# Kernel optimization log

Hardware: AMD Instinct MI355X
Metric: run time of the kernel (lower is better)

The kernel has to match this reference:

```python
import jax, jax.numpy as jnp
import numpy as np

N_HEAD = 8
HEAD_DIM = 128
WINDOW = 512
ROPE_BASE = 10000.0


def _rope_tables(T, dtype):
    # inv_freq: [head_dim/2]
    inv_freq = 1.0 / (ROPE_BASE ** (jnp.arange(0, HEAD_DIM, 2, dtype=jnp.float32) / HEAD_DIM))
    t = jnp.arange(T, dtype=jnp.float32)
    freqs = jnp.einsum('i,j->ij', t, inv_freq)          # [T, head_dim/2]
    emb = jnp.concatenate([freqs, freqs], axis=-1)       # [T, head_dim]
    return jnp.cos(emb).astype(dtype), jnp.sin(emb).astype(dtype)


def _rotate_half(x):
    d = x.shape[-1] // 2
    return jnp.concatenate([-x[..., d:], x[..., :d]], axis=-1)


def setup_inputs() -> dict:
    key = jax.random.key(0)
    k1, k2, k3 = jax.random.split(key, 3)
    B, T, C = 2, 4096, 1024
    x = jax.random.normal(k1, (B, T, C), dtype=jnp.float32)
    w_qkv = jax.random.normal(k2, (3 * C, C), dtype=jnp.float32) * (1.0 / np.sqrt(C))
    w_o = jax.random.normal(k3, (C, C), dtype=jnp.float32) * (1.0 / np.sqrt(C))
    return {"x": x, "w_qkv": w_qkv, "w_o": w_o}


def reference(x, w_qkv, w_o):
    B, T, C = x.shape
    scale = 1.0 / np.sqrt(HEAD_DIM)
    qkv = x @ w_qkv.T                                     # [B,T,3C]
    q, k, v = jnp.split(qkv, 3, axis=-1)
    # [B, H, T, D]
    q = q.reshape(B, T, N_HEAD, HEAD_DIM).transpose(0, 2, 1, 3)
    k = k.reshape(B, T, N_HEAD, HEAD_DIM).transpose(0, 2, 1, 3)
    v = v.reshape(B, T, N_HEAD, HEAD_DIM).transpose(0, 2, 1, 3)
    cos, sin = _rope_tables(T, x.dtype)                   # [T, D]
    cos = cos[None, None]
    sin = sin[None, None]
    q = q * cos + _rotate_half(q) * sin
    k = k * cos + _rotate_half(k) * sin
    attn = jnp.einsum('bhqd,bhkd->bhqk', q, k) * scale    # [B,H,T,T]
    i = jnp.arange(T)[:, None]
    j = jnp.arange(T)[None, :]
    # causal (j<=i) AND sliding window triu(diag=-W) (j >= i - W)
    keep = (j <= i) & (j >= i - WINDOW)
    neg = jnp.finfo(attn.dtype).min
    attn = jnp.where(keep[None, None], attn, neg)
    attn = jax.nn.softmax(attn, axis=-1)
    out = jnp.einsum('bhqk,bhkd->bhqd', attn, v)          # [B,H,T,D]
    out = out.transpose(0, 2, 1, 3).reshape(B, T, C)
    return out @ w_o.T
```

## Files before the change

kernel.cpp:

```cpp
#include <hip/hip_runtime.h>
#include <hip/hip_bf16.h>

typedef unsigned short us;
typedef __attribute__((ext_vector_type(8))) __bf16 bf16x8;
typedef __attribute__((ext_vector_type(4))) float f32x4;

#define MFMA16(a, b, c) __builtin_amdgcn_mfma_f32_16x16x32_bf16(a, b, c, 0, 0, 0)

static __device__ __forceinline__ us f2bf(float f) {
  __hip_bfloat16 h = __float2bfloat16(f);
  return __builtin_bit_cast(us, h);
}

static __device__ __forceinline__ void gll16(const us* g, us* l) {
  __builtin_amdgcn_global_load_lds((const __attribute__((address_space(1))) void*)g,
                                   (__attribute__((address_space(3))) void*)l,
                                   16, 0, 0);
}

__global__ void prep_kernel(const float* __restrict__ x, const float* __restrict__ wq,
                            const float* __restrict__ wo, us* __restrict__ xb,
                            us* __restrict__ wqb, us* __restrict__ wob,
                            float* __restrict__ ct, float* __restrict__ st) {
  const int blk = blockIdx.x;
  const int tid = threadIdx.x;
  if (blk < 12288) {
    const float* in;
    us* out;
    int i;
    if (blk < 8192)      { in = x;  out = xb;  i = blk * 256 + tid; }
    else if (blk < 11264){ in = wq; out = wqb; i = (blk - 8192) * 256 + tid; }
    else                 { in = wo; out = wob; i = (blk - 11264) * 256 + tid; }
    float4 v = ((const float4*)in)[i];
    ushort4 o;
    o.x = f2bf(v.x); o.y = f2bf(v.y); o.z = f2bf(v.z); o.w = f2bf(v.w);
    ((ushort4*)out)[i] = o;
  } else {
    int i = (blk - 12288) * 256 + tid;
    int t = i >> 6, d = i & 63;
    float ang = (float)t * exp2f((float)d * -0.20762050593046014f);
    float s, c;
    sincosf(ang, &s, &c);
    ct[i] = c;
    st[i] = s;
  }
}

__global__ __launch_bounds__(256, 4)
void qkv_rope_kernel(const us* __restrict__ A, const us* __restrict__ B,
                     const float* __restrict__ ctab, const float* __restrict__ stab,
                     us* __restrict__ qb, us* __restrict__ kb, us* __restrict__ vtb) {
  __shared__ __align__(16) char smem_raw[128 * 136 * 2];
  us* sA = (us*)smem_raw;
  us* sB = sA + 128 * 64;
  us* sCus = (us*)smem_raw;

  const int tid = threadIdx.x;
  const int lane = tid & 63;
  const int wave = tid >> 6;
  const int l15 = lane & 15;
  const int lq = lane >> 4;
  const int m0 = blockIdx.x * 128;
  const int n0 = blockIdx.y * 128;
  const int wm = (wave & 1) * 64;
  const int wn2 = (wave >> 1) * 32;

  f32x4 acc[4][4] = {};

  for (int k0 = 0; k0 < 1024; k0 += 64) {
    for (int i = 0; i < 4; ++i) {
      int c = wave * 4 + i;
      int P = c * 64 + lane;
      int row = P >> 3;
      int cb = (P & 7) ^ (row & 7);
      gll16(A + (size_t)(m0 + row) * 1024 + k0 + cb * 8, sA + c * 512);
      gll16(B + (size_t)(n0 + row) * 1024 + k0 + cb * 8, sB + c * 512);
    }
    __syncthreads();
#pragma unroll
    for (int kk = 0; kk < 64; kk += 32) {
      const int cbr = (kk + lq * 8) >> 3;
      bf16x8 av[4], bv[4];
#pragma unroll
      for (int mt = 0; mt < 4; ++mt) {
        int m = wm + mt * 16 + l15;
        av[mt] = *(const bf16x8*)(sA + (m * 8 + (cbr ^ (m & 7))) * 8);
      }
#pragma unroll
      for (int nt = 0; nt < 4; ++nt) {
        int n = wn2 + (nt & 1) * 16 + (nt >> 1) * 64 + l15;
        bv[nt] = *(const bf16x8*)(sB + (n * 8 + (cbr ^ (n & 7))) * 8);
      }
#pragma unroll
      for (int mt = 0; mt < 4; ++mt)
#pragma unroll
        for (int nt = 0; nt < 4; ++nt)
          acc[mt][nt] = MFMA16(av[mt], bv[nt], acc[mt][nt]);
    }
    __syncthreads();
  }

  const int b = m0 >> 12;
  const int t0 = m0 & 4095;
  const int which = blockIdx.y >> 3;
  const int h = blockIdx.y & 7;

  if (which < 2) {
    us* outp = (which == 0) ? qb : kb;
    const size_t obase = ((size_t)(b * 8 + h)) * 4096 * 128;
#pragma unroll
    for (int mt = 0; mt < 4; ++mt)
#pragma unroll
      for (int r = 0; r < 4; ++r) {
        const int row = wm + mt * 16 + lq * 4 + r;
        const int tg = t0 + row;
        const float* cp = ctab + tg * 64 + wn2 + l15;
        const float* sp = stab + tg * 64 + wn2 + l15;
        const float c0 = cp[0], c1 = cp[16], s0 = sp[0], s1 = sp[16];
#pragma unroll
        for (int nt = 0; nt < 4; ++nt) {
          float xv = acc[mt][nt][r];
          float xp = acc[mt][nt ^ 2][r];
          float rot = (nt < 2) ? -xp : xp;
          float y = xv * ((nt & 1) ? c1 : c0) + rot * ((nt & 1) ? s1 : s0);
          sCus[row * 136 + wn2 + (nt & 1) * 16 + (nt >> 1) * 64 + l15] = f2bf(y);
        }
      }
    __syncthreads();
    for (int r = 0; r < 8; ++r) {
      int row = (tid >> 4) + r * 16;
      int col = (tid & 15) * 8;
      uint4 v = *(const uint4*)(sCus + row * 136 + col);
      *(uint4*)(outp + obase + (size_t)(t0 + row) * 128 + col) = v;
    }
  } else {
#pragma unroll
    for (int mt = 0; mt < 4; ++mt)
#pragma unroll
      for (int nt = 0; nt < 4; ++nt) {
        const int col = wn2 + (nt & 1) * 16 + (nt >> 1) * 64 + l15;
#pragma unroll
        for (int r = 0; r < 4; ++r)
          sCus[(wm + mt * 16 + lq * 4 + r) * 130 + col] = f2bf(acc[mt][nt][r]);
      }
    __syncthreads();
    for (int r = 0; r < 8; ++r) {
      int d = (tid >> 4) + r * 16;
      int tl0 = (tid & 15) * 8;
      union { us u[8]; uint4 v; } tmp;
#pragma unroll
      for (int j = 0; j < 8; ++j)
        tmp.u[j] = sCus[(tl0 + j) * 130 + d];
      *(uint4*)(vtb + ((size_t)((b * 8 + h) * 128 + d)) * 4096 + t0 + tl0) = tmp.v;
    }
  }
}

template <int MASK>
__device__ __forceinline__ void p_write(f32x4 (&s)[2][4], us* __restrict__ sP,
                                        int t0, int tj0, int wm2, int lq, int l15) {
  const float C2 = 0.08838834764831845f * 1.4426950408889634f;
#pragma unroll
  for (int mt = 0; mt < 2; ++mt)
#pragma unroll
    for (int nt = 0; nt < 4; ++nt) {
      const int jg = tj0 + nt * 16 + l15;
      const int cb = (nt * 16 + l15) >> 3;
      const int co = l15 & 7;
#pragma unroll
      for (int r = 0; r < 4; ++r) {
        const int rowl = wm2 + mt * 16 + lq * 4 + r;
        float v = s[mt][nt][r];
        if (MASK == 1) v = (jg + 512 >= t0 + rowl) ? v : -3.0e38f;
        if (MASK == 2) v = (jg <= t0 + rowl) ? v : -3.0e38f;
        sP[rowl * 64 + ((cb ^ (rowl & 7)) * 8) + co] = f2bf(exp2f(v * C2));
      }
    }
}

__global__ __launch_bounds__(256, 2)
void flash_kernel(const us* __restrict__ qg, const us* __restrict__ kg,
                  const us* __restrict__ vg, us* __restrict__ ao) {
  __shared__ us smem[40960];
  us* sK = smem;
  us* sV = smem + 16384;
  us* sP = smem + 32768;

  const int tid = threadIdx.x;
  const int lane = tid & 63;
  const int wave = tid >> 6;
  const int l15 = lane & 15;
  const int lq = lane >> 4;
  const int qx = blockIdx.x;
  const int h = blockIdx.y;
  const int b = blockIdx.z;
  const int t0 = qx * 128;
  const size_t bh = (size_t)(b * 8 + h);
  const int wm2 = wave * 32;

  bf16x8 qf[2][4];
#pragma unroll
  for (int mt = 0; mt < 2; ++mt)
#pragma unroll
    for (int ks = 0; ks < 4; ++ks)
      qf[mt][ks] = *(const bf16x8*)(qg + (bh * 4096 + t0 + wm2 + mt * 16 + l15) * 128 +
                                    ks * 32 + lq * 8);

  union { us u[8]; bf16x8 v; } one_u;
#pragma unroll
  for (int i = 0; i < 8; ++i) one_u.u[i] = 0x3F80;
  const bf16x8 vone = one_u.v;

  f32x4 o[2][9] = {};

  const int lo = t0 - 512;
  const int jtmin = (lo <= 0) ? 0 : (lo >> 6);
  const int jtmax = (t0 + 127) >> 6;
  const bool wmask = (t0 >= 512);

  auto stage = [&](int jt, int buf) {
    const int tj0 = jt * 64;
    us* dK = sK + buf * 8192;
    us* dV = sV + buf * 8192;
    for (int i = 0; i < 4; ++i) {
      int c = wave * 4 + i;
      int P = c * 64 + lane;
      int rowK = P >> 4;
      int cbK = (P & 15) ^ (rowK & 15);
      gll16(kg + (bh * 4096 + tj0 + rowK) * 128 + cbK * 8, dK + c * 512);
      int rowV = P >> 3;
      int cbV = (P & 7) ^ (rowV & 7);
      gll16(vg + (bh * 128 + rowV) * 4096 + tj0 + cbV * 8, dV + c * 512);
    }
  };

  stage(jtmin, 0);
  int cur = 0;

  for (int jt = jtmin; jt <= jtmax; ++jt) {
    __syncthreads();
    if (jt < jtmax) stage(jt + 1, cur ^ 1);

    const int tj0 = jt * 64;
    const us* sKc = sK + cur * 8192;
    const us* sVc = sV + cur * 8192;

    f32x4 s[2][4] = {};
#pragma unroll
    for (int ks = 0; ks < 4; ++ks) {
      const int cbr = ks * 4 + lq;
#pragma unroll
      for (int nt = 0; nt < 4; ++nt) {
        int n = nt * 16 + l15;
        bf16x8 bk = *(const bf16x8*)(sKc + (n * 16 + (cbr ^ (n & 15))) * 8);
#pragma unroll
        for (int mt = 0; mt < 2; ++mt)
          s[mt][nt] = MFMA16(qf[mt][ks], bk, s[mt][nt]);
      }
    }

    if (jt >= jtmax - 1)               p_write<2>(s, sP, t0, tj0, wm2, lq, l15);
    else if (wmask && jt <= jtmin + 1) p_write<1>(s, sP, t0, tj0, wm2, lq, l15);
    else                               p_write<0>(s, sP, t0, tj0, wm2, lq, l15);

#pragma unroll
    for (int ks = 0; ks < 2; ++ks) {
#pragma unroll
      for (int mt = 0; mt < 2; ++mt) {
        bf16x8 ap = *(const bf16x8*)(sP + (wm2 + mt * 16 + l15) * 64 +
                                     (((ks * 4 + lq) ^ (l15 & 7)) * 8));
#pragma unroll
        for (int dt = 0; dt < 8; ++dt) {
          int dd = dt * 16 + l15;
          bf16x8 bv = *(const bf16x8*)(sVc + (dd * 8 + ((ks * 4 + lq) ^ (dd & 7))) * 8);
          o[mt][dt] = MFMA16(ap, bv, o[mt][dt]);
        }
        o[mt][8] = MFMA16(ap, vone, o[mt][8]);
      }
    }
    cur ^= 1;
  }

#pragma unroll
  for (int mt = 0; mt < 2; ++mt)
#pragma unroll
    for (int r = 0; r < 4; ++r) {
      const float inv = 1.0f / o[mt][8][r];
      const int rowl = wm2 + mt * 16 + lq * 4 + r;
      const size_t base = ((size_t)b * 4096 + t0 + rowl) * 1024 + h * 128;
#pragma unroll
      for (int dt = 0; dt < 8; ++dt)
        ao[base + dt * 16 + l15] = f2bf(o[mt][dt][r] * inv);
    }
}

__global__ __launch_bounds__(256, 2)
void out_proj_kernel(const us* __restrict__ A, const us* __restrict__ B, float* __restrict__ C) {
  __shared__ us sA[128 * 64];
  __shared__ us sB[128 * 64];
  const int tid = threadIdx.x;
  const int lane = tid & 63;
  const int wave = tid >> 6;
  const int l15 = lane & 15;
  const int lq = lane >> 4;
  const int m0 = blockIdx.x * 128;
  const int n0 = blockIdx.y * 128;
  const int wm = (wave & 1) * 64;
  const int wn = (wave >> 1) * 64;
  f32x4 acc[4][4] = {};
  for (int k0 = 0; k0 < 1024; k0 += 64) {
    for (int i = 0; i < 4; ++i) {
      int c = wave * 4 + i;
      int P = c * 64 + lane;
      int row = P >> 3;
      int cb = (P & 7) ^ (row & 7);
      gll16(A + (size_t)(m0 + row) * 1024 + k0 + cb * 8, sA + c * 512);
      gll16(B + (size_t)(n0 + row) * 1024 + k0 + cb * 8, sB + c * 512);
    }
    __syncthreads();
#pragma unroll
    for (int kk = 0; kk < 64; kk += 32) {
      const int cbr = (kk + lq * 8) >> 3;
      bf16x8 av[4], bv[4];
#pragma unroll
      for (int mt = 0; mt < 4; ++mt) {
        int m = wm + mt * 16 + l15;
        av[mt] = *(const bf16x8*)(sA + (m * 8 + (cbr ^ (m & 7))) * 8);
      }
#pragma unroll
      for (int nt = 0; nt < 4; ++nt) {
        int n = wn + nt * 16 + l15;
        bv[nt] = *(const bf16x8*)(sB + (n * 8 + (cbr ^ (n & 7))) * 8);
      }
#pragma unroll
      for (int mt = 0; mt < 4; ++mt)
#pragma unroll
        for (int nt = 0; nt < 4; ++nt)
          acc[mt][nt] = MFMA16(av[mt], bv[nt], acc[mt][nt]);
    }
    __syncthreads();
  }
#pragma unroll
  for (int mt = 0; mt < 4; ++mt)
#pragma unroll
    for (int nt = 0; nt < 4; ++nt)
#pragma unroll
      for (int r = 0; r < 4; ++r)
        C[(size_t)(m0 + wm + mt * 16 + lq * 4 + r) * 1024 + (n0 + wn + nt * 16 + l15)] =
            acc[mt][nt][r];
}

extern "C" void kernel_launch(void* const* d_in, const int* in_sizes, int n_in,
                              void* d_out, int out_size, void* d_ws, size_t ws_size,
                              hipStream_t stream) {
  const float* x     = (const float*)d_in[0];
  const float* w_qkv = (const float*)d_in[1];
  const float* w_o   = (const float*)d_in[2];
  float* out = (float*)d_out;

  us* xb  = (us*)d_ws;
  us* wqb = xb  + (size_t)8192 * 1024;
  us* wob = wqb + (size_t)3072 * 1024;
  us* qb  = wob + (size_t)1024 * 1024;
  us* kb  = qb  + (size_t)2 * 8 * 4096 * 128;
  us* vtb = kb  + (size_t)2 * 8 * 4096 * 128;
  us* aob = vtb + (size_t)2 * 8 * 4096 * 128;
  float* ctab = (float*)(aob + (size_t)8192 * 1024);
  float* stab = ctab + (size_t)4096 * 64;

  prep_kernel<<<13312, 256, 0, stream>>>(x, w_qkv, w_o, xb, wqb, wob, ctab, stab);
  qkv_rope_kernel<<<dim3(64, 24), 256, 0, stream>>>(xb, wqb, ctab, stab, qb, kb, vtb);
  flash_kernel<<<dim3(32, 8, 2), 256, 0, stream>>>(qb, kb, vtb, aob);
  out_proj_kernel<<<dim3(64, 8), 256, 0, stream>>>(aob, wob, out);
}
```

Baseline: 206.7 us.

## Shrink flash query tile to 64 rows and drop K/V double buffering

The flash kernel now handles 64 query rows per block instead of 128, with 16 rows per wave, and launches twice as many blocks. The K/V double buffer is removed, which halves LDS use and lets launch bounds request 4 blocks per CU for more occupancy and parallelism. In exchange, each K/V tile is loaded synchronously with an extra barrier and no prefetch overlap. Each block also reuses a K/V tile over fewer query rows, so more total K/V traffic goes through global memory.

```diff
diff --git a/kernel.cpp b/kernel.cpp
--- a/kernel.cpp
+++ b/kernel.cpp
@@ -157,34 +157,32 @@
 }
 
 template <int MASK>
-__device__ __forceinline__ void p_write(f32x4 (&s)[2][4], us* __restrict__ sP,
+__device__ __forceinline__ void p_write(f32x4 (&s)[4], us* __restrict__ sP,
                                         int t0, int tj0, int wm2, int lq, int l15) {
   const float C2 = 0.08838834764831845f * 1.4426950408889634f;
 #pragma unroll
-  for (int mt = 0; mt < 2; ++mt)
-#pragma unroll
-    for (int nt = 0; nt < 4; ++nt) {
-      const int jg = tj0 + nt * 16 + l15;
-      const int cb = (nt * 16 + l15) >> 3;
-      const int co = l15 & 7;
-#pragma unroll
-      for (int r = 0; r < 4; ++r) {
-        const int rowl = wm2 + mt * 16 + lq * 4 + r;
-        float v = s[mt][nt][r];
-        if (MASK == 1) v = (jg + 512 >= t0 + rowl) ? v : -3.0e38f;
-        if (MASK == 2) v = (jg <= t0 + rowl) ? v : -3.0e38f;
-        sP[rowl * 64 + ((cb ^ (rowl & 7)) * 8) + co] = f2bf(exp2f(v * C2));
-      }
-    }
-}
-
-__global__ __launch_bounds__(256, 2)
+  for (int nt = 0; nt < 4; ++nt) {
+    const int jg = tj0 + nt * 16 + l15;
+    const int cb = (nt * 16 + l15) >> 3;
+    const int co = l15 & 7;
+#pragma unroll
+    for (int r = 0; r < 4; ++r) {
+      const int rowl = wm2 + lq * 4 + r;
+      float v = s[nt][r];
+      if (MASK == 1) v = (jg + 512 >= t0 + rowl) ? v : -3.0e38f;
+      if (MASK == 2) v = (jg <= t0 + rowl) ? v : -3.0e38f;
+      sP[rowl * 64 + ((cb ^ (rowl & 7)) * 8) + co] = f2bf(exp2f(v * C2));
+    }
+  }
+}
+
+__global__ __launch_bounds__(256, 4)
 void flash_kernel(const us* __restrict__ qg, const us* __restrict__ kg,
                   const us* __restrict__ vg, us* __restrict__ ao) {
-  __shared__ us smem[40960];
+  __shared__ us smem[20480];
   us* sK = smem;
-  us* sV = smem + 16384;
-  us* sP = smem + 32768;
+  us* sV = smem + 8192;
+  us* sP = smem + 16384;
 
   const int tid = threadIdx.x;
   const int lane = tid & 63;
@@ -194,104 +192,88 @@
   const int qx = blockIdx.x;
   const int h = blockIdx.y;
   const int b = blockIdx.z;
-  const int t0 = qx * 128;
+  const int t0 = qx * 64;
   const size_t bh = (size_t)(b * 8 + h);
-  const int wm2 = wave * 32;
-
-  bf16x8 qf[2][4];
-#pragma unroll
-  for (int mt = 0; mt < 2; ++mt)
-#pragma unroll
-    for (int ks = 0; ks < 4; ++ks)
-      qf[mt][ks] = *(const bf16x8*)(qg + (bh * 4096 + t0 + wm2 + mt * 16 + l15) * 128 +
-                                    ks * 32 + lq * 8);
+  const int wm2 = wave * 16;
+
+  bf16x8 qf[4];
+#pragma unroll
+  for (int ks = 0; ks < 4; ++ks)
+    qf[ks] = *(const bf16x8*)(qg + (bh * 4096 + t0 + wm2 + l15) * 128 +
+                              ks * 32 + lq * 8);
 
   union { us u[8]; bf16x8 v; } one_u;
 #pragma unroll
   for (int i = 0; i < 8; ++i) one_u.u[i] = 0x3F80;
   const bf16x8 vone = one_u.v;
 
-  f32x4 o[2][9] = {};
+  f32x4 o[9] = {};
 
   const int lo = t0 - 512;
   const int jtmin = (lo <= 0) ? 0 : (lo >> 6);
-  const int jtmax = (t0 + 127) >> 6;
+  const int jtmax = t0 >> 6;
   const bool wmask = (t0 >= 512);
 
-  auto stage = [&](int jt, int buf) {
+  auto stage = [&](int jt) {
     const int tj0 = jt * 64;
-    us* dK = sK + buf * 8192;
-    us* dV = sV + buf * 8192;
     for (int i = 0; i < 4; ++i) {
       int c = wave * 4 + i;
       int P = c * 64 + lane;
       int rowK = P >> 4;
       int cbK = (P & 15) ^ (rowK & 15);
-      gll16(kg + (bh * 4096 + tj0 + rowK) * 128 + cbK * 8, dK + c * 512);
+      gll16(kg + (bh * 4096 + tj0 + rowK) * 128 + cbK * 8, sK + c * 512);
       int rowV = P >> 3;
       int cbV = (P & 7) ^ (rowV & 7);
-      gll16(vg + (bh * 128 + rowV) * 4096 + tj0 + cbV * 8, dV + c * 512);
+      gll16(vg + (bh * 128 + rowV) * 4096 + tj0 + cbV * 8, sV + c * 512);
     }
   };
 
-  stage(jtmin, 0);
-  int cur = 0;
-
   for (int jt = jtmin; jt <= jtmax; ++jt) {
     __syncthreads();
-    if (jt < jtmax) stage(jt + 1, cur ^ 1);
+    stage(jt);
+    __syncthreads();
 
     const int tj0 = jt * 64;
-    const us* sKc = sK + cur * 8192;
-    const us* sVc = sV + cur * 8192;
-
-    f32x4 s[2][4] = {};
+
+    f32x4 s[4] = {};
 #pragma unroll
     for (int ks = 0; ks < 4; ++ks) {
       const int cbr = ks * 4 + lq;
 #pragma unroll
       for (int nt = 0; nt < 4; ++nt) {
         int n = nt * 16 + l15;
-        bf16x8 bk = *(const bf16x8*)(sKc + (n * 16 + (cbr ^ (n & 15))) * 8);
-#pragma unroll
-        for (int mt = 0; mt < 2; ++mt)
-          s[mt][nt] = MFMA16(qf[mt][ks], bk, s[mt][nt]);
-      }
-    }
-
-    if (jt >= jtmax - 1)               p_write<2>(s, sP, t0, tj0, wm2, lq, l15);
-    else if (wmask && jt <= jtmin + 1) p_write<1>(s, sP, t0, tj0, wm2, lq, l15);
-    else                               p_write<0>(s, sP, t0, tj0, wm2, lq, l15);
+        bf16x8 bk = *(const bf16x8*)(sK + (n * 16 + (cbr ^ (n & 15))) * 8);
+        s[nt] = MFMA16(qf[ks], bk, s[nt]);
+      }
+    }
+
+    if (jt == jtmax)                p_write<2>(s, sP, t0, tj0, wm2, lq, l15);
+    else if (wmask && jt == jtmin)  p_write<1>(s, sP, t0, tj0, wm2, lq, l15);
+    else                            p_write<0>(s, sP, t0, tj0, wm2, lq, l15);
 
 #pragma unroll
     for (int ks = 0; ks < 2; ++ks) {
-#pragma unroll
-      for (int mt = 0; mt < 2; ++mt) {
-        bf16x8 ap = *(const bf16x8*)(sP + (wm2 + mt * 16 + l15) * 64 +
-                                     (((ks * 4 + lq) ^ (l15 & 7)) * 8));
-#pragma unroll
-        for (int dt = 0; dt < 8; ++dt) {
-          int dd = dt * 16 + l15;
-          bf16x8 bv = *(const bf16x8*)(sVc + (dd * 8 + ((ks * 4 + lq) ^ (dd & 7))) * 8);
-          o[mt][dt] = MFMA16(ap, bv, o[mt][dt]);
-        }
-        o[mt][8] = MFMA16(ap, vone, o[mt][8]);
-      }
-    }
-    cur ^= 1;
-  }
-
-#pragma unroll
-  for (int mt = 0; mt < 2; ++mt)
-#pragma unroll
-    for (int r = 0; r < 4; ++r) {
-      const float inv = 1.0f / o[mt][8][r];
-      const int rowl = wm2 + mt * 16 + lq * 4 + r;
-      const size_t base = ((size_t)b * 4096 + t0 + rowl) * 1024 + h * 128;
-#pragma unroll
-      for (int dt = 0; dt < 8; ++dt)
-        ao[base + dt * 16 + l15] = f2bf(o[mt][dt][r] * inv);
-    }
+      bf16x8 ap = *(const bf16x8*)(sP + (wm2 + l15) * 64 +
+                                   (((ks * 4 + lq) ^ (l15 & 7)) * 8));
+#pragma unroll
+      for (int dt = 0; dt < 8; ++dt) {
+        int dd = dt * 16 + l15;
+        bf16x8 bv = *(const bf16x8*)(sV + (dd * 8 + ((ks * 4 + lq) ^ (dd & 7))) * 8);
+        o[dt] = MFMA16(ap, bv, o[dt]);
+      }
+      o[8] = MFMA16(ap, vone, o[8]);
+    }
+  }
+
+#pragma unroll
+  for (int r = 0; r < 4; ++r) {
+    const float inv = 1.0f / o[8][r];
+    const int rowl = wm2 + lq * 4 + r;
+    const size_t base = ((size_t)b * 4096 + t0 + rowl) * 1024 + h * 128;
+#pragma unroll
+    for (int dt = 0; dt < 8; ++dt)
+      ao[base + dt * 16 + l15] = f2bf(o[dt][r] * inv);
+  }
 }
 
 __global__ __launch_bounds__(256, 2)
@@ -370,6 +352,6 @@
 
   prep_kernel<<<13312, 256, 0, stream>>>(x, w_qkv, w_o, xb, wqb, wob, ctab, stab);
   qkv_rope_kernel<<<dim3(64, 24), 256, 0, stream>>>(xb, wqb, ctab, stab, qb, kb, vtb);
-  flash_kernel<<<dim3(32, 8, 2), 256, 0, stream>>>(qb, kb, vtb, aob);
+  flash_kernel<<<dim3(64, 8, 2), 256, 0, stream>>>(qb, kb, vtb, aob);
   out_proj_kernel<<<dim3(64, 8), 256, 0, stream>>>(aob, wob, out);
 }
```

Measured after the change: 248.6 us. 1.2x slower.
